# Kernel tuning notes

Hardware: AMD Instinct MI355X
Metric: run time of the kernel (lower is better)

The kernel has to match this reference:

```python
import jax, jax.numpy as jnp
import numpy as np

B, S, D = 2, 2048, 2048          # batch, max_seq_len, hidden_dim_attention
G, HPG = 8, 4                    # n_head_groups, n_heads_per_group
H = G * HPG                      # total heads = 32
HD = D // H                      # head_dim = 64
KV = D // G                      # kv projection dim = 256
DFF = 5632                       # hidden_dim_feedforward
EPS = 1e-6
SCALE = 1.0 / (jnp.sqrt(jnp.float32(D // G)) + EPS)  # sqrt(attention_dim // n_head_groups) + eps


def setup_inputs() -> dict:
    key = jax.random.key(0)
    ks = jax.random.split(key, 12)
    s = lambda fan_in: 1.0 / np.sqrt(fan_in)
    return {
        "x": jax.random.normal(ks[0], (B, S, D), jnp.float32),
        "position_matrix": jax.random.uniform(ks[1], (2, 1, S, D), jnp.float32),
        "norm_attn_w": jnp.ones((D,), jnp.float32),
        "norm_ff_w": jnp.ones((D,), jnp.float32),
        "wq": jax.random.normal(ks[2], (D, D), jnp.float32) * s(D),
        "wk": jax.random.normal(ks[3], (KV, D), jnp.float32) * s(D),
        "wv": jax.random.normal(ks[4], (KV, D), jnp.float32) * s(D),
        "wo": jax.random.normal(ks[5], (D, D), jnp.float32) * s(D),
        "gate_w": jax.random.normal(ks[6], (DFF, D), jnp.float32) * s(D),
        "up_w": jax.random.normal(ks[7], (DFF, D), jnp.float32) * s(D),
        "down_w": jax.random.normal(ks[8], (DFF, D).__class__((D, DFF)), jnp.float32) * s(DFF),
    }


def rmsnorm(x, w):
    xf = x.astype(jnp.float32)
    n = xf / (jnp.sqrt(jnp.mean(xf * xf, axis=-1, keepdims=True) + EPS) + EPS)
    return n.astype(x.dtype) * w


def embed_position(x, pm):
    # faithful to source: rotated half times (cos + sin) tables (source multiplies _x by both)
    d = x.shape[-1]
    _x = jnp.concatenate((-x[..., d // 2:], x[..., :d // 2]), axis=-1)
    return (_x * pm[0][:, :, :d] + _x * pm[1][:, :, :d]).astype(x.dtype)


def block(x, position_matrix, norm_attn_w, norm_ff_w, wq, wk, wv, wo, gate_w, up_w, down_w):
    # ---- attention sublayer ----
    h = rmsnorm(x, norm_attn_w)
    xq = h @ wq.T                                   # [B,S,D]
    xk = h @ wk.T                                   # [B,S,KV]
    xv = h @ wv.T                                   # [B,S,KV]
    xq = embed_position(xq, position_matrix)
    xk = embed_position(xk, position_matrix)
    # GQA broadcast: each group's KV dims split into HPG heads of HD
    xk = jnp.broadcast_to(xk[:, :, None, :], (B, S, G, KV)).reshape(B, S, H, HD).transpose(0, 2, 1, 3)
    xv = jnp.broadcast_to(xv[:, :, None, :], (B, S, G, KV)).reshape(B, S, H, HD).transpose(0, 2, 1, 3)
    xq = xq.reshape(B, S, H, HD).transpose(0, 2, 1, 3)  # [B,H,S,HD]
    score = jnp.einsum("bhqd,bhkd->bhqk", xq, xk) * SCALE
    # source mask: strictly-upper triangle filled with 1e-10 (added, not -inf) -- faithful
    mask = jnp.triu(jnp.full((S, S), 1e-10, jnp.float32), k=1)
    score = score + mask
    e = jnp.exp(score.astype(jnp.float32))
    attn = (e / (jnp.sum(e, axis=-1, keepdims=True) + 1.0)).astype(xq.dtype)
    out = jnp.einsum("bhqk,bhkd->bhqd", attn, xv)
    out = out.transpose(0, 2, 1, 3).reshape(B, S, D) @ wo.T
    x = x + out
    # ---- feedforward sublayer (SwiGLU) ----
    h2 = rmsnorm(x, norm_ff_w)
    ff = (jax.nn.silu(h2 @ gate_w.T) * (h2 @ up_w.T)) @ down_w.T
    return x + ff


def reference(x, position_matrix, norm_attn_w, norm_ff_w, wq, wk, wv, wo, gate_w, up_w, down_w):
    return block(x, position_matrix, norm_attn_w, norm_ff_w, wq, wk, wv, wo, gate_w, up_w, down_w)
```

## Files before the change

kernel.cpp:

```cpp
#include <hip/hip_runtime.h>


typedef __attribute__((ext_vector_type(8))) __bf16 bf16x8;
typedef __attribute__((ext_vector_type(4))) __bf16 bf16x4;
typedef __attribute__((ext_vector_type(4))) float f32x4;

#define RR 4096
#define DD 2048
#define KVD 256
#define QKVN 2560
#define DFF 5632

static const size_t OFF_WQKV = 0;
static const size_t OFF_WO   = 10485760;
static const size_t OFF_WG   = 18874368;
static const size_t OFF_WU   = 41943040;
static const size_t OFF_WDN  = 65011712;
static const size_t OFF_H    = 88080384;
static const size_t OFF_QKV  = 104857600;
static const size_t OFF_Q    = 125829120;
static const size_t OFF_K    = 142606336;
static const size_t OFF_ACT  = 144703488;
static const size_t WS_NEED  = 190840832;

__device__ __forceinline__ void glds16(const __bf16* g, __bf16* s) {
  __builtin_amdgcn_global_load_lds(
      (const __attribute__((address_space(1))) unsigned int*)(const void*)g,
      (__attribute__((address_space(3))) unsigned int*)(void*)s, 16, 0, 0);
}

__global__ void cvt_kernel(const float* __restrict__ s, __bf16* __restrict__ d, int n4) {
  int i = blockIdx.x * 256 + threadIdx.x;
  if (i >= n4) return;
  float4 v = ((const float4*)s)[i];
  union { __bf16 b[4]; ushort4 u; } c;
  c.b[0] = (__bf16)v.x; c.b[1] = (__bf16)v.y; c.b[2] = (__bf16)v.z; c.b[3] = (__bf16)v.w;
  ((ushort4*)d)[i] = c.u;
}

__global__ __launch_bounds__(256)
void rmsnorm_kernel(const float* __restrict__ x, const float* __restrict__ w,
                    __bf16* __restrict__ out) {
  const int row = blockIdx.x, t = threadIdx.x;
  const float4* xr = (const float4*)(x + (size_t)row * DD);
  float4 a = xr[t], b = xr[t + 256];
  float s = a.x*a.x + a.y*a.y + a.z*a.z + a.w*a.w
          + b.x*b.x + b.y*b.y + b.z*b.z + b.w*b.w;
#pragma unroll
  for (int m = 1; m < 64; m <<= 1) s += __shfl_xor(s, m, 64);
  __shared__ float red[4];
  if ((t & 63) == 0) red[t >> 6] = s;
  __syncthreads();
  float tot = red[0] + red[1] + red[2] + red[3];
  float inv = 1.0f / (sqrtf(tot * (1.0f / 2048.0f) + 1e-6f) + 1e-6f);
  const float4* wr = (const float4*)w;
  float4 w0 = wr[t], w1 = wr[t + 256];
  __bf16* o = out + (size_t)row * DD;
  union { __bf16 bb[4]; ushort4 u; } c;
  c.bb[0] = (__bf16)(a.x*inv*w0.x); c.bb[1] = (__bf16)(a.y*inv*w0.y);
  c.bb[2] = (__bf16)(a.z*inv*w0.z); c.bb[3] = (__bf16)(a.w*inv*w0.w);
  ((ushort4*)o)[t] = c.u;
  c.bb[0] = (__bf16)(b.x*inv*w1.x); c.bb[1] = (__bf16)(b.y*inv*w1.y);
  c.bb[2] = (__bf16)(b.z*inv*w1.z); c.bb[3] = (__bf16)(b.w*inv*w1.w);
  ((ushort4*)o)[t + 256] = c.u;
}

template<int EPI>
__global__ __launch_bounds__(256)
void gemm_nt_kernel(const __bf16* __restrict__ A, const __bf16* __restrict__ Bm,
                    __bf16* Cb, const float* __restrict__ Res,
                    float* __restrict__ Cf, int M, int N, int K) {
  __shared__ __align__(16) __bf16 As[128 * 64];
  __shared__ __align__(16) __bf16 Bs[128 * 64];
  const int t = threadIdx.x;
  const int GM = M >> 7, GN = N >> 7;
  int m_t, n_t;
  if (GM == 32 && (GN & 3) == 0) {
    int lid = blockIdx.y * gridDim.x + blockIdx.x;
    int xcd = lid & 7, i = lid >> 3;
    int c = i >> 4, j = i & 15;
    m_t = xcd * 4 + (j & 3);
    n_t = c * 4 + (j >> 2);
  } else {
    m_t = blockIdx.y; n_t = blockIdx.x;
  }
  const int m0 = m_t * 128, n0 = n_t * 128;
  const int w = t >> 6, l = t & 63;
  const int wm = w & 1, wn = w >> 1;
  const int lm = l & 15, lq = l >> 4;
  const int srow = w * 8 + (l >> 3);
  const int sslot = (l & 7) ^ (l >> 3);
  const __bf16* Ap = A + (size_t)(m0 + srow) * K + sslot * 8;
  const __bf16* Bp = Bm + (size_t)(n0 + srow) * K + sslot * 8;
  __bf16* AsW = As + w * 512;
  __bf16* BsW = Bs + w * 512;
  const int sl0 = ((lq) ^ (lm & 7)) << 3;
  const int sl1 = ((4 + lq) ^ (lm & 7)) << 3;
  f32x4 acc[4][4] = {};
  for (int kt = 0; kt < K; kt += 64) {
    __syncthreads();
#pragma unroll
    for (int it = 0; it < 4; it++) {
      glds16(Ap + (size_t)(it * 32) * K + kt, AsW + it * 2048);
      glds16(Bp + (size_t)(it * 32) * K + kt, BsW + it * 2048);
    }
    __syncthreads();
    bf16x8 af[2][4], bfr[2][4];
#pragma unroll
    for (int i = 0; i < 4; i++) {
      af[0][i]  = *(const bf16x8*)&As[(wm * 64 + i * 16 + lm) * 64 + sl0];
      af[1][i]  = *(const bf16x8*)&As[(wm * 64 + i * 16 + lm) * 64 + sl1];
      bfr[0][i] = *(const bf16x8*)&Bs[(wn * 64 + i * 16 + lm) * 64 + sl0];
      bfr[1][i] = *(const bf16x8*)&Bs[(wn * 64 + i * 16 + lm) * 64 + sl1];
    }
#pragma unroll
    for (int kk = 0; kk < 2; kk++)
#pragma unroll
      for (int i = 0; i < 4; i++)
#pragma unroll
        for (int j = 0; j < 4; j++)
          acc[i][j] = __builtin_amdgcn_mfma_f32_16x16x32_bf16(af[kk][i], bfr[kk][j], acc[i][j], 0, 0, 0);
  }
#pragma unroll
  for (int i = 0; i < 4; i++)
#pragma unroll
    for (int j = 0; j < 4; j++)
#pragma unroll
      for (int r = 0; r < 4; r++) {
        int row = m0 + wm * 64 + i * 16 + lq * 4 + r;
        int col = n0 + wn * 64 + j * 16 + lm;
        size_t idx = (size_t)row * N + col;
        if (EPI == 0) {
          Cb[idx] = (__bf16)acc[i][j][r];
        } else if (EPI == 1) {
          Cf[idx] = Res[idx] + acc[i][j][r];
        } else {
          float g = (float)Cb[idx];
          Cb[idx] = (__bf16)(g / (1.0f + __expf(-g)) * acc[i][j][r]);
        }
      }
}

__global__ __launch_bounds__(256)
void rope_kernel(const __bf16* __restrict__ qkv, const float* __restrict__ pm,
                 __bf16* __restrict__ qo, __bf16* __restrict__ ko) {
  const int row = blockIdx.x, t = threadIdx.x;
  const int s = row & 2047;
  const __bf16* q = qkv + (size_t)row * QKVN;
  const float* p0 = pm + (size_t)s * DD;
  const float* p1 = p0 + (size_t)2048 * DD;
  __bf16* qr = qo + (size_t)row * DD;
#pragma unroll
  for (int jj = 0; jj < 8; jj++) {
    int i = t + jj * 256;
    float rot = (i < 1024) ? -(float)q[i + 1024] : (float)q[i - 1024];
    qr[i] = (__bf16)(rot * (p0[i] + p1[i]));
  }
  const __bf16* k = q + 2048;
  __bf16* kr = ko + (size_t)row * KVD;
  {
    int i = t;
    float rot = (i < 128) ? -(float)k[i + 128] : (float)k[i - 128];
    kr[i] = (__bf16)(rot * (p0[i] + p1[i]));
  }
}

__global__ __launch_bounds__(256)
void attn_kernel(const __bf16* __restrict__ Q, const __bf16* __restrict__ Kb,
                 const __bf16* __restrict__ QKV, __bf16* __restrict__ O) {
  __shared__ __align__(16) __bf16 sQ[128 * 72];
  __shared__ __align__(16) __bf16 sK[64 * 72];
  __shared__ __align__(16) __bf16 sV[64 * 72];
  __shared__ float sDen[128];
  const int t = threadIdx.x, l = t & 63, w = t >> 6;
  const int lm = l & 15, lq = l >> 4;
  const int q0 = blockIdx.x * 128;
  const int h = blockIdx.y, b = blockIdx.z;
  const int p = h & 3;
  const float scale = 1.0f / (16.0f + 1e-6f);
  {
    const int qr = t >> 3, qc = (t & 7) * 8;
#pragma unroll
    for (int it = 0; it < 4; it++) {
      size_t base = ((size_t)(b * 2048 + q0 + qr + it * 32)) * DD + h * 64 + qc;
      *(uint4*)&sQ[(qr + it * 32) * 72 + qc] = *(const uint4*)(Q + base);
    }
  }
  f32x4 oacc[2][4] = {};
  float dsum[2] = {0.f, 0.f};
  const int ksr = t >> 2, ksc = (t & 3) * 16;
  for (int kt = 0; kt < 2048; kt += 64) {
    const __bf16* krow = Kb + ((size_t)(b * 2048 + kt + ksr)) * KVD + p * 64 + ksc;
    uint4 kv0 = *(const uint4*)(krow);
    uint4 kv1 = *(const uint4*)(krow + 8);
    unsigned int vpack[8];
    {
      const __bf16* vbase = QKV + ((size_t)(b * 2048 + kt + w * 16)) * QKVN + 2304 + p * 64 + l;
#pragma unroll
      for (int j2 = 0; j2 < 8; j2++) {
        unsigned int u0 = *(const unsigned short*)(vbase + (size_t)(2 * j2) * QKVN);
        unsigned int u1 = *(const unsigned short*)(vbase + (size_t)(2 * j2 + 1) * QKVN);
        vpack[j2] = u0 | (u1 << 16);
      }
    }
    __syncthreads();
    *(uint4*)&sK[ksr * 72 + ksc] = kv0;
    *(uint4*)&sK[ksr * 72 + ksc + 8] = kv1;
    *(uint4*)&sV[l * 72 + w * 16] = *(uint4*)&vpack[0];
    *(uint4*)&sV[l * 72 + w * 16 + 8] = *(uint4*)&vpack[4];
    __syncthreads();
    bf16x8 bQ[2][2];
#pragma unroll
    for (int q_j = 0; q_j < 2; q_j++)
#pragma unroll
      for (int kk = 0; kk < 2; kk++)
        bQ[q_j][kk] = *(const bf16x8*)&sQ[(w * 32 + q_j * 16 + lm) * 72 + kk * 32 + lq * 8];
#pragma unroll
    for (int kt2 = 0; kt2 < 2; kt2++) {
      union { bf16x8 v; __bf16 e[8]; } pA[2];
#pragma unroll
      for (int c = 0; c < 2; c++) {
        const int kt_i = kt2 * 2 + c;
        f32x4 sacc[2] = {};
#pragma unroll
        for (int kk = 0; kk < 2; kk++) {
          bf16x8 aK = *(const bf16x8*)&sK[(kt_i * 16 + lm) * 72 + kk * 32 + lq * 8];
#pragma unroll
          for (int q_j = 0; q_j < 2; q_j++)
            sacc[q_j] = __builtin_amdgcn_mfma_f32_16x16x32_bf16(aK, bQ[q_j][kk], sacc[q_j], 0, 0, 0);
        }
#pragma unroll
        for (int q_j = 0; q_j < 2; q_j++)
#pragma unroll
          for (int r = 0; r < 4; r++) {
            float e = __expf(sacc[q_j][r] * scale);
            dsum[q_j] += e;
            pA[q_j].e[c * 4 + r] = (__bf16)e;
          }
      }
#pragma unroll
      for (int d_n = 0; d_n < 4; d_n++) {
        union { bf16x8 v; bf16x4 h[2]; } bV;
        const __bf16* vb = &sV[(d_n * 16 + lm) * 72 + kt2 * 32 + lq * 4];
        bV.h[0] = *(const bf16x4*)(vb);
        bV.h[1] = *(const bf16x4*)(vb + 16);
#pragma unroll
        for (int q_j = 0; q_j < 2; q_j++)
          oacc[q_j][d_n] = __builtin_amdgcn_mfma_f32_16x16x32_bf16(pA[q_j].v, bV.v, oacc[q_j][d_n], 0, 0, 0);
      }
    }
  }
#pragma unroll
  for (int q_j = 0; q_j < 2; q_j++) {
    dsum[q_j] += __shfl_xor(dsum[q_j], 16, 64);
    dsum[q_j] += __shfl_xor(dsum[q_j], 32, 64);
  }
  if (l < 16) {
    sDen[w * 32 + l] = dsum[0];
    sDen[w * 32 + 16 + l] = dsum[1];
  }
  __syncthreads();
#pragma unroll
  for (int q_j = 0; q_j < 2; q_j++)
#pragma unroll
    for (int d_n = 0; d_n < 4; d_n++)
#pragma unroll
      for (int r = 0; r < 4; r++) {
        int rloc = w * 32 + q_j * 16 + lq * 4 + r;
        int row = q0 + rloc;
        int col = h * 64 + d_n * 16 + lm;
        O[((size_t)(b * 2048 + row)) * DD + col] = (__bf16)(oacc[q_j][d_n][r] / (sDen[rloc] + 1.0f));
      }
}

extern "C" void kernel_launch(void* const* d_in, const int* in_sizes, int n_in,
                              void* d_out, int out_size, void* d_ws, size_t ws_size,
                              hipStream_t stream) {
  if (ws_size < WS_NEED) return;

  const float* x    = (const float*)d_in[0];
  const float* pm   = (const float*)d_in[1];
  const float* w_na = (const float*)d_in[2];
  const float* w_nf = (const float*)d_in[3];
  const float* wq   = (const float*)d_in[4];
  const float* wk   = (const float*)d_in[5];
  const float* wv   = (const float*)d_in[6];
  const float* wo   = (const float*)d_in[7];
  const float* wg   = (const float*)d_in[8];
  const float* wu   = (const float*)d_in[9];
  const float* wd   = (const float*)d_in[10];

  char* ws = (char*)d_ws;
  __bf16* wqkv_b = (__bf16*)(ws + OFF_WQKV);
  __bf16* wo_b   = (__bf16*)(ws + OFF_WO);
  __bf16* wg_b   = (__bf16*)(ws + OFF_WG);
  __bf16* wu_b   = (__bf16*)(ws + OFF_WU);
  __bf16* wdn_b  = (__bf16*)(ws + OFF_WDN);
  __bf16* h_b    = (__bf16*)(ws + OFF_H);
  __bf16* qkv_b  = (__bf16*)(ws + OFF_QKV);
  __bf16* q_b    = (__bf16*)(ws + OFF_Q);
  __bf16* k_b    = (__bf16*)(ws + OFF_K);
  __bf16* act_b  = (__bf16*)(ws + OFF_ACT);
  float*  x1     = (float*)d_out;

  cvt_kernel<<<4096, 256, 0, stream>>>(wq, wqkv_b, 1048576);
  cvt_kernel<<<512, 256, 0, stream>>>(wk, wqkv_b + (size_t)2048 * 2048, 131072);
  cvt_kernel<<<512, 256, 0, stream>>>(wv, wqkv_b + (size_t)2304 * 2048, 131072);
  cvt_kernel<<<4096, 256, 0, stream>>>(wo, wo_b, 1048576);
  cvt_kernel<<<11264, 256, 0, stream>>>(wg, wg_b, 2883584);
  cvt_kernel<<<11264, 256, 0, stream>>>(wu, wu_b, 2883584);
  cvt_kernel<<<11264, 256, 0, stream>>>(wd, wdn_b, 2883584);

  rmsnorm_kernel<<<4096, 256, 0, stream>>>(x, w_na, h_b);
  gemm_nt_kernel<0><<<dim3(20, 32), 256, 0, stream>>>(h_b, wqkv_b, qkv_b, nullptr, nullptr,
                                                      RR, QKVN, DD);
  rope_kernel<<<4096, 256, 0, stream>>>(qkv_b, pm, q_b, k_b);
  attn_kernel<<<dim3(16, 32, 2), 256, 0, stream>>>(q_b, k_b, qkv_b, h_b);
  gemm_nt_kernel<1><<<dim3(16, 32), 256, 0, stream>>>(h_b, wo_b, nullptr, x, x1,
                                                      RR, DD, DD);
  rmsnorm_kernel<<<4096, 256, 0, stream>>>(x1, w_nf, q_b);
  gemm_nt_kernel<0><<<dim3(44, 32), 256, 0, stream>>>(q_b, wg_b, act_b, nullptr, nullptr,
                                                      RR, DFF, DD);
  gemm_nt_kernel<2><<<dim3(44, 32), 256, 0, stream>>>(q_b, wu_b, act_b, nullptr, nullptr,
                                                      RR, DFF, DD);
  gemm_nt_kernel<1><<<dim3(16, 32), 256, 0, stream>>>(act_b, wdn_b, nullptr, x1, x1,
                                                      RR, DD, DFF);
}
```

Before: 894.9 us.

## Fuse gate/up GEMMs into one SwiGLU kernel and merge weight conversions

Replaces the separate gate and up projection GEMMs with one kernel that loads the A tile once, computes both gate and up accumulators, and applies SiLU-multiply in the epilogue. This removes the intermediate bf16 gate write/read and one pass over the normalized activations. It also merges seven weight-conversion launches into one kernel. The new kernel uses 512 threads and three shared buffers with a custom block-to-tile mapping, which changes occupancy and scheduling behavior.

```diff
diff --git a/kernel.cpp b/kernel.cpp
--- a/kernel.cpp
+++ b/kernel.cpp
@@ -29,13 +29,26 @@
       (__attribute__((address_space(3))) unsigned int*)(void*)s, 16, 0, 0);
 }
 
-__global__ void cvt_kernel(const float* __restrict__ s, __bf16* __restrict__ d, int n4) {
+__global__ __launch_bounds__(256)
+void cvt_all_kernel(const float* __restrict__ wq, const float* __restrict__ wk,
+                    const float* __restrict__ wv, const float* __restrict__ wo,
+                    const float* __restrict__ wg, const float* __restrict__ wu,
+                    const float* __restrict__ wd, __bf16* __restrict__ wqkv,
+                    __bf16* __restrict__ wob, __bf16* __restrict__ wgb,
+                    __bf16* __restrict__ wub, __bf16* __restrict__ wdb) {
   int i = blockIdx.x * 256 + threadIdx.x;
-  if (i >= n4) return;
-  float4 v = ((const float4*)s)[i];
+  const float* s; __bf16* d; int si, di;
+  if (i < 1048576)      { s = wq; d = wqkv; si = i;           di = i; }
+  else if (i < 1179648) { s = wk; d = wqkv; si = i - 1048576; di = i; }
+  else if (i < 1310720) { s = wv; d = wqkv; si = i - 1179648; di = i; }
+  else if (i < 2359296) { s = wo; d = wob;  si = i - 1310720; di = si; }
+  else if (i < 5242880) { s = wg; d = wgb;  si = i - 2359296; di = si; }
+  else if (i < 8126464) { s = wu; d = wub;  si = i - 5242880; di = si; }
+  else                  { s = wd; d = wdb;  si = i - 8126464; di = si; }
+  float4 v = ((const float4*)s)[si];
   union { __bf16 b[4]; ushort4 u; } c;
   c.b[0] = (__bf16)v.x; c.b[1] = (__bf16)v.y; c.b[2] = (__bf16)v.z; c.b[3] = (__bf16)v.w;
-  ((ushort4*)d)[i] = c.u;
+  ((ushort4*)d)[di] = c.u;
 }
 
 __global__ __launch_bounds__(256)
@@ -132,12 +145,78 @@
         size_t idx = (size_t)row * N + col;
         if (EPI == 0) {
           Cb[idx] = (__bf16)acc[i][j][r];
-        } else if (EPI == 1) {
+        } else {
           Cf[idx] = Res[idx] + acc[i][j][r];
-        } else {
-          float g = (float)Cb[idx];
-          Cb[idx] = (__bf16)(g / (1.0f + __expf(-g)) * acc[i][j][r]);
         }
+      }
+}
+
+__global__ __launch_bounds__(512)
+void gemm_glu_kernel(const __bf16* __restrict__ A, const __bf16* __restrict__ Gm,
+                     const __bf16* __restrict__ Um, __bf16* __restrict__ Cb,
+                     int M, int N, int K) {
+  __shared__ __align__(16) __bf16 As[128 * 64];
+  __shared__ __align__(16) __bf16 Gs[128 * 64];
+  __shared__ __align__(16) __bf16 Us[128 * 64];
+  const int t = threadIdx.x, w = t >> 6, l = t & 63;
+  const int lm = l & 15, lq = l >> 4;
+  const int wm = w >> 2, wn = w & 3;
+  const int lid = blockIdx.y * gridDim.x + blockIdx.x;
+  const int xcd = lid & 7, i0 = lid >> 3;
+  const int cc = i0 >> 4, jj0 = i0 & 15;
+  const int m0 = (xcd * 4 + (jj0 & 3)) * 128;
+  const int n0 = (cc * 4 + (jj0 >> 2)) * 128;
+  const int srow = w * 8 + (l >> 3);
+  const int sslot = (l & 7) ^ (l >> 3);
+  const __bf16* Ap = A + (size_t)(m0 + srow) * K + sslot * 8;
+  const __bf16* Gp = Gm + (size_t)(n0 + srow) * K + sslot * 8;
+  const __bf16* Up = Um + (size_t)(n0 + srow) * K + sslot * 8;
+  __bf16* AsW = As + w * 512;
+  __bf16* GsW = Gs + w * 512;
+  __bf16* UsW = Us + w * 512;
+  const int sl0 = ((lq) ^ (lm & 7)) << 3;
+  const int sl1 = ((4 + lq) ^ (lm & 7)) << 3;
+  f32x4 accg[4][2] = {}, accu[4][2] = {};
+  for (int kt = 0; kt < K; kt += 64) {
+    __syncthreads();
+    glds16(Ap + kt, AsW);
+    glds16(Ap + (size_t)64 * K + kt, AsW + 4096);
+    glds16(Gp + kt, GsW);
+    glds16(Gp + (size_t)64 * K + kt, GsW + 4096);
+    glds16(Up + kt, UsW);
+    glds16(Up + (size_t)64 * K + kt, UsW + 4096);
+    __syncthreads();
+#pragma unroll
+    for (int kk = 0; kk < 2; kk++) {
+      const int sl = kk ? sl1 : sl0;
+      bf16x8 af[4], bg[2], bu[2];
+#pragma unroll
+      for (int i = 0; i < 4; i++)
+        af[i] = *(const bf16x8*)&As[(wm * 64 + i * 16 + lm) * 64 + sl];
+#pragma unroll
+      for (int j = 0; j < 2; j++) {
+        bg[j] = *(const bf16x8*)&Gs[(wn * 32 + j * 16 + lm) * 64 + sl];
+        bu[j] = *(const bf16x8*)&Us[(wn * 32 + j * 16 + lm) * 64 + sl];
+      }
+#pragma unroll
+      for (int i = 0; i < 4; i++)
+#pragma unroll
+        for (int j = 0; j < 2; j++) {
+          accg[i][j] = __builtin_amdgcn_mfma_f32_16x16x32_bf16(af[i], bg[j], accg[i][j], 0, 0, 0);
+          accu[i][j] = __builtin_amdgcn_mfma_f32_16x16x32_bf16(af[i], bu[j], accu[i][j], 0, 0, 0);
+        }
+    }
+  }
+#pragma unroll
+  for (int i = 0; i < 4; i++)
+#pragma unroll
+    for (int j = 0; j < 2; j++)
+#pragma unroll
+      for (int r = 0; r < 4; r++) {
+        int row = m0 + wm * 64 + i * 16 + lq * 4 + r;
+        int col = n0 + wn * 32 + j * 16 + lm;
+        float g = accg[i][j][r];
+        Cb[(size_t)row * N + col] = (__bf16)(g / (1.0f + __expf(-g)) * accu[i][j][r]);
       }
 }
 
@@ -303,13 +382,8 @@
   __bf16* act_b  = (__bf16*)(ws + OFF_ACT);
   float*  x1     = (float*)d_out;
 
-  cvt_kernel<<<4096, 256, 0, stream>>>(wq, wqkv_b, 1048576);
-  cvt_kernel<<<512, 256, 0, stream>>>(wk, wqkv_b + (size_t)2048 * 2048, 131072);
-  cvt_kernel<<<512, 256, 0, stream>>>(wv, wqkv_b + (size_t)2304 * 2048, 131072);
-  cvt_kernel<<<4096, 256, 0, stream>>>(wo, wo_b, 1048576);
-  cvt_kernel<<<11264, 256, 0, stream>>>(wg, wg_b, 2883584);
-  cvt_kernel<<<11264, 256, 0, stream>>>(wu, wu_b, 2883584);
-  cvt_kernel<<<11264, 256, 0, stream>>>(wd, wdn_b, 2883584);
+  cvt_all_kernel<<<43008, 256, 0, stream>>>(wq, wk, wv, wo, wg, wu, wd,
+                                            wqkv_b, wo_b, wg_b, wu_b, wdn_b);
 
   rmsnorm_kernel<<<4096, 256, 0, stream>>>(x, w_na, h_b);
   gemm_nt_kernel<0><<<dim3(20, 32), 256, 0, stream>>>(h_b, wqkv_b, qkv_b, nullptr, nullptr,
@@ -319,10 +393,8 @@
   gemm_nt_kernel<1><<<dim3(16, 32), 256, 0, stream>>>(h_b, wo_b, nullptr, x, x1,
                                                       RR, DD, DD);
   rmsnorm_kernel<<<4096, 256, 0, stream>>>(x1, w_nf, q_b);
-  gemm_nt_kernel<0><<<dim3(44, 32), 256, 0, stream>>>(q_b, wg_b, act_b, nullptr, nullptr,
-                                                      RR, DFF, DD);
-  gemm_nt_kernel<2><<<dim3(44, 32), 256, 0, stream>>>(q_b, wu_b, act_b, nullptr, nullptr,
-                                                      RR, DFF, DD);
+  gemm_glu_kernel<<<dim3(44, 32), 512, 0, stream>>>(q_b, wg_b, wu_b, act_b,
+                                                    RR, DFF, DD);
   gemm_nt_kernel<1><<<dim3(16, 32), 256, 0, stream>>>(act_b, wdn_b, nullptr, x1, x1,
                                                       RR, DD, DFF);
 }
```

After: 799.1 us. 1.12x faster.
